# Optimization experiments

Measured on AMD Instinct MI355X. Metric: run time of the kernel, lower is better.

The kernel has to match this reference:

```python
import jax, jax.numpy as jnp
import numpy as np

K = 12           # Emb.k (piece types)
NKB = 4          # kNumKingBuckets
PIECE_DIM = K * 64

KING_BUCKETS = jnp.array([0,0,0,0,0,0,0,0, 0,0,0,0,0,0,0,0, 0,0,0,0,0,0,0,0, 0,0,0,0,0,0,0,0, 0,0,0,0,0,0,0,0, 0,0,0,0,0,0,0,0, 0,0,0,0,0,0,0,0, 3,3,0,0,1,0,2,2], dtype=jnp.int32)


def make_factorization_mask():
    m = np.ones((NKB, K, 8, 8, 1), np.float32)
    for p in (0, K // 2):
        m[:, p, 0, :, :] = 0.0
        m[:, p, 7, :, :] = 0.0
    return jnp.asarray(m)


def setup_inputs() -> dict:
    key = jax.random.key(0)
    ks = jax.random.split(key, 8)
    B, L, DOUT = 16384, 32, 128
    T = B * L
    s = (1.0 / 30.0) ** 0.5  # kRoughEstimateOfNumberOfOnesInInput ~ 30
    values = jax.random.randint(ks[0], (T,), 0, PIECE_DIM, dtype=jnp.int32)
    lengths = jnp.full((B,), L, dtype=jnp.int32)
    kings = jax.random.randint(ks[1], (B, 2), 0, 64, dtype=jnp.int32)
    pieces = jax.random.normal(ks[2], (NKB, K, 1, 1, DOUT), jnp.float32) * s
    ranks = jax.random.normal(ks[3], (NKB, K, 8, 1, DOUT), jnp.float32) * s
    files = jax.random.normal(ks[4], (NKB, K, 1, 8, DOUT), jnp.float32) * s
    noking = jax.random.normal(ks[5], (1, K, 8, 8, DOUT), jnp.float32) * s
    tiles = jax.random.normal(ks[6], (NKB, K, 8, 8, DOUT), jnp.float32) * s
    fmask = make_factorization_mask()
    return {"values": values, "lengths": lengths, "kings": kings,
            "pieces": pieces, "ranks": ranks, "files": files,
            "noking": noking, "tiles": tiles, "fmask": fmask}


def flip_values(v):
    piece = v // 64
    sq = v % 64
    return ((piece + K // 2) % K) * 64 + (7 - sq // 8) * 8 + sq % 8


def reference(values, lengths, kings, pieces, ranks, files, noking, tiles, fmask):
    B = lengths.shape[0]
    T = values.shape[0]
    dout = tiles.shape[-1]
    # merged tile table: (NKB, K, 8, 8, dout) -> (NKB*K*64, dout)
    merged = tiles + (pieces + ranks + files) * fmask + noking
    w = merged.reshape(NKB * K * 64, dout)
    mover_bucket = KING_BUCKETS[kings[:, 0]]
    wk = kings[:, 1]
    wk_flipped = (7 - wk // 8) * 8 + wk % 8
    waiter_bucket = KING_BUCKETS[wk_flipped]
    # expand per-board buckets to per-feature (lengths are static 32)
    mb = jnp.repeat(mover_bucket, lengths, total_repeat_length=T)
    wb = jnp.repeat(waiter_bucket, lengths, total_repeat_length=T)
    seg = jnp.repeat(jnp.arange(B, dtype=jnp.int32), lengths, total_repeat_length=T)
    mover_values = mb * PIECE_DIM + values
    waiter_values = wb * PIECE_DIM + flip_values(values)
    a = jax.ops.segment_sum(w[mover_values], seg, num_segments=B)
    b = jax.ops.segment_sum(w[waiter_values], seg, num_segments=B)
    return jnp.clip(a, 0.0, 1.0), jnp.clip(b, 0.0, 1.0)
```

## Files before the change

### kernel.cpp

```cpp
#include <hip/hip_runtime.h>

#define K 12
#define NKB 4
#define PIECE_DIM (K * 64)
#define NROWS (NKB * PIECE_DIM)
#define DOUT 128
#define BATCH 16384
#define SEQL 32

typedef float    f32x4 __attribute__((ext_vector_type(4)));
typedef _Float16 f16x4 __attribute__((ext_vector_type(4)));

__global__ __launch_bounds__(DOUT) void build_w_kernel(
    const float* __restrict__ pieces,
    const float* __restrict__ ranks,
    const float* __restrict__ files,
    const float* __restrict__ noking,
    const float* __restrict__ tiles,
    const float* __restrict__ fmask,
    _Float16* __restrict__ w)
{
    int row = blockIdx.x;
    int d   = threadIdx.x;
    int nkb = row / PIECE_DIM;
    int rem = row - nkb * PIECE_DIM;
    int k   = rem >> 6;
    int sq  = rem & 63;
    int r   = sq >> 3;
    int f   = sq & 7;
    int nk_k = nkb * K + k;

    float p  = pieces[nk_k * DOUT + d];
    float rk = ranks[(nk_k * 8 + r) * DOUT + d];
    float fl = files[(nk_k * 8 + f) * DOUT + d];
    float nk = noking[((k * 8 + r) * 8 + f) * DOUT + d];
    float tl = tiles[((nk_k * 8 + r) * 8 + f) * DOUT + d];
    float fm = fmask[(nk_k * 8 + r) * 8 + f];

    w[row * DOUT + d] = (_Float16)(tl + (p + rk + fl) * fm + nk);
}

__device__ __forceinline__ int king_bucket(int s) {
    const unsigned long long hi =
        (3ULL << 48) | (3ULL << 50) | (1ULL << 56) | (2ULL << 60) | (2ULL << 62);
    int t = s - 32;
    return (t >= 0) ? (int)((hi >> (2 * t)) & 3ULL) : 0;
}

__global__ __launch_bounds__(256) void gather_kernel(
    const int* __restrict__ values,
    const int* __restrict__ kings,
    const _Float16* __restrict__ w,
    float* __restrict__ out)
{
    int wave = threadIdx.x >> 6;
    int lane = threadIdx.x & 63;
    int b    = blockIdx.x * 4 + wave;
    int half = lane >> 5;
    int c    = lane & 31;

    int km   = kings[2 * b];
    int kw   = kings[2 * b + 1];
    int mbkt = king_bucket(km);
    int wbkt = king_bucket(kw ^ 56);
    int base = (half ? wbkt : mbkt) * PIECE_DIM;

    int xm = half ? 56 : 0;
    int am = half ? -1 : 0;
    int laneoff = (base << 8) + c * 8;

    const int4* vp = (const int4*)(values + b * SEQL);
    const char* wb = (const char*)w;

    f32x4 acc = (f32x4)(0.f);
    int4 cur = vp[0];

    #pragma unroll 1
    for (int j = 0; j < SEQL / 4; ++j) {
        int jn = (j < SEQL / 4 - 1) ? j + 1 : j;
        int4 nxt = vp[jn];
        int vs[4] = {cur.x, cur.y, cur.z, cur.w};
        #pragma unroll
        for (int u = 0; u < 4; ++u) {
            int v   = vs[u];
            int adj = ((v < 384) ? 384 : -384) & am;
            int rv  = (v ^ xm) + adj;
            unsigned off = (unsigned)(laneoff + (rv << 8));
            f16x4 x = *(const f16x4*)(wb + off);
            acc += __builtin_convertvector(x, f32x4);
        }
        cur = nxt;
    }

    acc.x = fminf(fmaxf(acc.x, 0.f), 1.f);
    acc.y = fminf(fmaxf(acc.y, 0.f), 1.f);
    acc.z = fminf(fmaxf(acc.z, 0.f), 1.f);
    acc.w = fminf(fmaxf(acc.w, 0.f), 1.f);

    f32x4* dst = (f32x4*)(out + (size_t)half * (BATCH * DOUT) + (size_t)b * DOUT) + c;
    __builtin_nontemporal_store(acc, dst);
}

extern "C" void kernel_launch(void* const* d_in, const int* in_sizes, int n_in,
                              void* d_out, int out_size, void* d_ws, size_t ws_size,
                              hipStream_t stream) {
    const int*   values = (const int*)d_in[0];
    const int*   kings  = (const int*)d_in[2];
    const float* pieces = (const float*)d_in[3];
    const float* ranks  = (const float*)d_in[4];
    const float* files  = (const float*)d_in[5];
    const float* noking = (const float*)d_in[6];
    const float* tiles  = (const float*)d_in[7];
    const float* fmask  = (const float*)d_in[8];

    _Float16* w   = (_Float16*)d_ws;
    float*    out = (float*)d_out;

    build_w_kernel<<<NROWS, DOUT, 0, stream>>>(pieces, ranks, files, noking,
                                               tiles, fmask, w);
    gather_kernel<<<BATCH / 4, 256, 0, stream>>>(values, kings, w, out);
}
```

Measured before the change: 98.57 us.

## Split sequence across lane quarters with 16-byte loads and cross-lane reduction

Result: faster. 89.83 us (-8.9%).

```diff
diff --git a/kernel.cpp b/kernel.cpp
--- a/kernel.cpp
+++ b/kernel.cpp
@@ -9,7 +9,8 @@
 #define SEQL 32
 
 typedef float    f32x4 __attribute__((ext_vector_type(4)));
-typedef _Float16 f16x4 __attribute__((ext_vector_type(4)));
+typedef float    f32x8 __attribute__((ext_vector_type(8)));
+typedef _Float16 f16x8 __attribute__((ext_vector_type(8)));
 
 __global__ __launch_bounds__(DOUT) void build_w_kernel(
     const float* __restrict__ pieces,
@@ -56,49 +57,56 @@
     int wave = threadIdx.x >> 6;
     int lane = threadIdx.x & 63;
     int b    = blockIdx.x * 4 + wave;
-    int half = lane >> 5;
-    int c    = lane & 31;
+    int q    = lane >> 4;
+    int c    = lane & 15;
+
+    int myv = values[b * SEQL + (lane & 31)];
 
     int km   = kings[2 * b];
     int kw   = kings[2 * b + 1];
     int mbkt = king_bucket(km);
     int wbkt = king_bucket(kw ^ 56);
-    int base = (half ? wbkt : mbkt) * PIECE_DIM;
 
-    int xm = half ? 56 : 0;
-    int am = half ? -1 : 0;
-    int laneoff = (base << 8) + c * 8;
+    const char* wbase = (const char*)w;
+    int moff = mbkt * (PIECE_DIM << 8) + c * 16;
+    int woff = wbkt * (PIECE_DIM << 8) + c * 16;
 
-    const int4* vp = (const int4*)(values + b * SEQL);
-    const char* wb = (const char*)w;
-
-    f32x4 acc = (f32x4)(0.f);
-    int4 cur = vp[0];
+    f32x8 accm = (f32x8)(0.f);
+    f32x8 accw = (f32x8)(0.f);
 
     #pragma unroll 1
     for (int j = 0; j < SEQL / 4; ++j) {
-        int jn = (j < SEQL / 4 - 1) ? j + 1 : j;
-        int4 nxt = vp[jn];
-        int vs[4] = {cur.x, cur.y, cur.z, cur.w};
-        #pragma unroll
-        for (int u = 0; u < 4; ++u) {
-            int v   = vs[u];
-            int adj = ((v < 384) ? 384 : -384) & am;
-            int rv  = (v ^ xm) + adj;
-            unsigned off = (unsigned)(laneoff + (rv << 8));
-            f16x4 x = *(const f16x4*)(wb + off);
-            acc += __builtin_convertvector(x, f32x4);
-        }
-        cur = nxt;
+        int v  = __shfl(myv, 4 * j + q, 64);
+        int fv = (v ^ 56) + ((v < 384) ? 384 : -384);
+        f16x8 xm = *(const f16x8*)(wbase + moff + (v  << 8));
+        f16x8 xw = *(const f16x8*)(wbase + woff + (fv << 8));
+        accm += __builtin_convertvector(xm, f32x8);
+        accw += __builtin_convertvector(xw, f32x8);
     }
 
-    acc.x = fminf(fmaxf(acc.x, 0.f), 1.f);
-    acc.y = fminf(fmaxf(acc.y, 0.f), 1.f);
-    acc.z = fminf(fmaxf(acc.z, 0.f), 1.f);
-    acc.w = fminf(fmaxf(acc.w, 0.f), 1.f);
+    #pragma unroll
+    for (int e = 0; e < 8; ++e) {
+        accm[e] += __shfl_xor(accm[e], 16, 64);
+        accm[e] += __shfl_xor(accm[e], 32, 64);
+        accw[e] += __shfl_xor(accw[e], 16, 64);
+        accw[e] += __shfl_xor(accw[e], 32, 64);
+        accm[e] = fminf(fmaxf(accm[e], 0.f), 1.f);
+        accw[e] = fminf(fmaxf(accw[e], 0.f), 1.f);
+    }
 
-    f32x4* dst = (f32x4*)(out + (size_t)half * (BATCH * DOUT) + (size_t)b * DOUT) + c;
-    __builtin_nontemporal_store(acc, dst);
+    if (q == 0) {
+        f32x4* dst = (f32x4*)(out + (size_t)b * DOUT + c * 8);
+        f32x4 lo = {accm[0], accm[1], accm[2], accm[3]};
+        f32x4 hi = {accm[4], accm[5], accm[6], accm[7]};
+        __builtin_nontemporal_store(lo, dst);
+        __builtin_nontemporal_store(hi, dst + 1);
+    } else if (q == 1) {
+        f32x4* dst = (f32x4*)(out + (size_t)(BATCH + b) * DOUT + c * 8);
+        f32x4 lo = {accw[0], accw[1], accw[2], accw[3]};
+        f32x4 hi = {accw[4], accw[5], accw[6], accw[7]};
+        __builtin_nontemporal_store(lo, dst);
+        __builtin_nontemporal_store(hi, dst + 1);
+    }
 }
 
 extern "C" void kernel_launch(void* const* d_in, const int* in_sizes, int n_in,
```
